# Optimization experiments

Measured on AMD Instinct MI355X. Metric: run time of the kernel, lower is better.

## Reference

```python
import jax, jax.numpy as jnp
import numpy as np

DIM = 768
H = 64
W = 64
NB = 8
BS = DIM // NB
LAMBD = 0.01
SCALE = 0.02


def softshrink(x, lambd):
    return jnp.sign(x) * jnp.maximum(jnp.abs(x) - lambd, 0.0)


def setup_inputs() -> dict:
    key = jax.random.key(0)
    ks = jax.random.split(key, 7)
    x = jax.random.normal(ks[0], (8, H * W, DIM), dtype=jnp.float32)
    w1 = SCALE * jax.random.normal(ks[1], (2, NB, BS, BS), dtype=jnp.float32)
    b1 = SCALE * jax.random.normal(ks[2], (2, NB, BS), dtype=jnp.float32)
    w2 = SCALE * jax.random.normal(ks[3], (2, NB, BS, BS), dtype=jnp.float32)
    b2 = SCALE * jax.random.normal(ks[4], (2, NB, BS), dtype=jnp.float32)
    # Conv1d(dim, dim, kernel_size=1) == per-token linear: weight [C_out, C_in], bias [C_out]
    Wb = (1.0 / np.sqrt(DIM)) * jax.random.normal(ks[5], (DIM, DIM), dtype=jnp.float32)
    bb = (1.0 / np.sqrt(DIM)) * jax.random.normal(ks[6], (DIM,), dtype=jnp.float32)
    return {"x": x, "w1": w1, "b1": b1, "w2": w2, "b2": b2, "Wb": Wb, "bb": bb}


def reference(x, w1, b1, w2, b2, Wb, bb):
    B, N, C = x.shape
    # bias path: Conv1d with kernel 1 is a linear map over channels
    bias = jnp.einsum('bnc,dc->bnd', x, Wb) + bb
    # spectral path
    xg = x.reshape(B, H, W, C)
    xf = jnp.fft.rfft2(xg, axes=(1, 2), norm='ortho')          # [B, H, W//2+1, C] complex64
    xf = xf.reshape(B, H, W // 2 + 1, NB, BS)
    xr, xi = jnp.real(xf), jnp.imag(xf)
    # layer 1: complex block-diagonal matmul + relu
    r1 = jax.nn.relu(jnp.einsum('...bd,bdk->...bk', xr, w1[0])
                     - jnp.einsum('...bd,bdk->...bk', xi, w1[1]) + b1[0])
    i1 = jax.nn.relu(jnp.einsum('...bd,bdk->...bk', xr, w1[1])
                     + jnp.einsum('...bd,bdk->...bk', xi, w1[0]) + b1[1])
    # layer 2
    r2 = (jnp.einsum('...bd,bdk->...bk', r1, w2[0])
          - jnp.einsum('...bd,bdk->...bk', i1, w2[1]) + b2[0])
    i2 = (jnp.einsum('...bd,bdk->...bk', r1, w2[1])
          + jnp.einsum('...bd,bdk->...bk', i1, w2[0]) + b2[1])
    r2 = softshrink(r2, LAMBD)
    i2 = softshrink(i2, LAMBD)
    xc = (r2 + 1j * i2).reshape(B, H, W // 2 + 1, C)
    xo = jnp.fft.irfft2(xc, s=(H, W), axes=(1, 2), norm='ortho')  # [B, H, W, C]
    return xo.reshape(B, N, C) + bias
```

## Files before the change

kernel.cpp:

```cpp
#include <hip/hip_runtime.h>
#include <math.h>

#ifndef M_PI
#define M_PI 3.14159265358979323846
#endif

namespace {

constexpr int kDim = 768;
constexpr int kNKW = 33;
constexpr int kB = 8;
constexpr float kLambd = 0.01f;
constexpr size_t kXFElems = (size_t)kB * kNKW * 64 * kDim;

typedef __attribute__((ext_vector_type(8))) __bf16 bf16x8;
typedef __attribute__((ext_vector_type(8))) short short8;
typedef __attribute__((ext_vector_type(4))) float f32x4;

alignas(16) __device__ unsigned short g_wT[4 * 8 * 96 * 96];
alignas(16) __device__ unsigned short g_twC[64 * 64];
alignas(16) __device__ unsigned short g_twS[64 * 64];
alignas(16) __device__ unsigned short g_iwC[64 * 64];
alignas(16) __device__ unsigned short g_iwS[64 * 64];

__device__ inline unsigned short f2bf(float f) {
  unsigned int u = __float_as_uint(f);
  unsigned int r = (u + 0x7FFFu + ((u >> 16) & 1u)) >> 16;
  return (unsigned short)r;
}

__device__ inline bf16x8 s2b(short8 s) { return __builtin_bit_cast(bf16x8, s); }
__device__ inline bf16x8 negb(short8 s) {
  s ^= (short)0x8000;
  return __builtin_bit_cast(bf16x8, s);
}

__device__ inline void gload_lds16(const void* g, void* l) {
  __builtin_amdgcn_global_load_lds(
      (const __attribute__((address_space(1))) unsigned int*)g,
      (__attribute__((address_space(3))) unsigned int*)l, 16, 0, 0);
}

__global__ __launch_bounds__(256) void init_tables_kernel() {
  const int e = blockIdx.x * 256 + threadIdx.x;
  if (e >= 4096) return;
  const int a = e >> 6;
  const int bcol = e & 63;
  const float ang = (float)(2.0 * M_PI / 64.0) * (float)((a * bcol) & 63);
  float s_, c_;
  __sincosf(ang, &s_, &c_);
  g_twC[e] = f2bf(0.125f * c_);
  g_twS[e] = f2bf(0.125f * s_);
  unsigned short cv = 0, sv = 0;
  if (bcol < 33) {
    const float al = (bcol == 0 || bcol == 32) ? 0.125f : 0.25f;
    cv = f2bf(al * c_);
    sv = f2bf(-al * s_);
  }
  g_iwC[e] = cv;
  g_iwS[e] = sv;
}

__global__ __launch_bounds__(256) void cvt_f32_bf16_kernel(
    const float* __restrict__ in, unsigned short* __restrict__ out, int n4) {
  int i = blockIdx.x * 256 + threadIdx.x;
  if (i >= n4) return;
  const float4 v = reinterpret_cast<const float4*>(in)[i];
  ushort4 o;
  o.x = f2bf(v.x); o.y = f2bf(v.y); o.z = f2bf(v.z); o.w = f2bf(v.w);
  reinterpret_cast<ushort4*>(out)[i] = o;
}

__global__ __launch_bounds__(256) void cvt_w_kernel(
    const float* __restrict__ w1, const float* __restrict__ w2) {
  const int e = blockIdx.x * 256 + threadIdx.x;
  if (e >= 4 * 8 * 96 * 96) return;
  const int k = e % 96;
  const int d = (e / 96) % 96;
  const int nbm = e / 9216;
  const int mtx = nbm >> 3;
  const int nb = nbm & 7;
  const float* src =
      (mtx < 2 ? w1 : w2) + ((size_t)(mtx & 1) * 8 + nb) * 9216;
  g_wT[((size_t)nbm * 96 + k) * 96 + d] = f2bf(src[d * 96 + k]);
}

__global__ __launch_bounds__(256) void mfma_gemm_kernel(
    const unsigned short* __restrict__ xbf, const unsigned short* __restrict__ wbf,
    const float* __restrict__ bb, float* __restrict__ out) {
  __shared__ unsigned short As[128 * 32];
  __shared__ unsigned short Bs[128 * 32];
  const int t = threadIdx.x;
  const int lane = t & 63;
  const int wid = t >> 6;
  const int wm = wid >> 1;
  const int wn = wid & 1;
  const int id = blockIdx.x;
  const int swz = (id & 7) * 192 + (id >> 3);
  const int m0 = (swz / 6) * 128;
  const int n0 = (swz % 6) * 128;

  f32x4 acc[4][4];
#pragma unroll
  for (int i = 0; i < 4; ++i)
#pragma unroll
    for (int j = 0; j < 4; ++j) acc[i][j] = (f32x4){0.f, 0.f, 0.f, 0.f};

  char* AsB = (char*)As;
  char* BsB = (char*)Bs;
  const int cl = lane & 15;
  const int kg = lane >> 4;

  for (int k0 = 0; k0 < 768; k0 += 32) {
#pragma unroll
    for (int i = 0; i < 2; ++i) {
      const int off = (wid * 2 + i) * 1024 + lane * 16;
      const int row = off >> 6;
      const int kb = off & 63;
      const char* gA = (const char*)xbf + ((size_t)(m0 + row) * 768 + k0) * 2 + kb;
      gload_lds16(gA, AsB + (wid * 2 + i) * 1024);
      const char* gB = (const char*)wbf + ((size_t)(n0 + row) * 768 + k0) * 2 + kb;
      gload_lds16(gB, BsB + (wid * 2 + i) * 1024);
    }
    asm volatile("s_waitcnt vmcnt(0)" ::: "memory");
    __syncthreads();

    bf16x8 av[4], bv[4];
#pragma unroll
    for (int mi = 0; mi < 4; ++mi) {
      const int r = wm * 64 + mi * 16 + cl;
      av[mi] = *reinterpret_cast<const bf16x8*>(AsB + r * 64 + kg * 16);
    }
#pragma unroll
    for (int ni = 0; ni < 4; ++ni) {
      const int r = wn * 64 + ni * 16 + cl;
      bv[ni] = *reinterpret_cast<const bf16x8*>(BsB + r * 64 + kg * 16);
    }
#pragma unroll
    for (int mi = 0; mi < 4; ++mi)
#pragma unroll
      for (int ni = 0; ni < 4; ++ni)
        acc[mi][ni] = __builtin_amdgcn_mfma_f32_16x16x32_bf16(
            av[mi], bv[ni], acc[mi][ni], 0, 0, 0);
    __syncthreads();
  }

#pragma unroll
  for (int ni = 0; ni < 4; ++ni) {
    const int n = n0 + wn * 64 + ni * 16 + cl;
    const float bias = bb[n];
#pragma unroll
    for (int mi = 0; mi < 4; ++mi) {
      const int m = m0 + wm * 64 + mi * 16 + kg * 4;
#pragma unroll
      for (int r = 0; r < 4; ++r) {
        out[(size_t)(m + r) * 768 + n] = acc[mi][ni][r] + bias;
      }
    }
  }
}

__global__ __launch_bounds__(256) void rfft_row_mfma_kernel(
    const float* __restrict__ x, unsigned short* __restrict__ xbf,
    unsigned short* __restrict__ XFr, unsigned short* __restrict__ XFi) {
  __shared__ alignas(16) unsigned short Cs[48 * 80];
  __shared__ alignas(16) unsigned short Ss[48 * 80];
  __shared__ alignas(16) unsigned short xs[64 * 66];
  const int t = threadIdx.x;
  for (int e = t; e < 48 * 64; e += 256) {
    const int kh = e >> 6;
    const int w = e & 63;
    const float ang = (float)(2.0 * M_PI / 64.0) * (float)((kh * w) & 63);
    float s_, c_;
    __sincosf(ang, &s_, &c_);
    Cs[kh * 80 + w] = f2bf(0.125f * c_);
    Ss[kh * 80 + w] = f2bf(-0.125f * s_);
  }

  const int lane = t & 63;
  const int wv = t >> 6;
  const int cl = lane & 15;
  const int kg = lane >> 4;
  const int bh = blockIdx.x;
  const int b = bh >> 6;
  const int h = bh & 63;
  const int c0 = blockIdx.y * 64;

  {
    const float* xrow = x + (size_t)bh * (64 * 768) + c0;
    unsigned short* xbrow = xbf + (size_t)bh * (64 * 768) + c0;
    const int wofs = lane >> 5;
    const int c2 = (lane & 31) * 2;
#pragma unroll
    for (int it = 0; it < 8; ++it) {
      const int w = wv * 16 + it * 2 + wofs;
      const float2 v = *reinterpret_cast<const float2*>(xrow + (size_t)w * 768 + c2);
      ushort2 bv;
      bv.x = f2bf(v.x);
      bv.y = f2bf(v.y);
      *reinterpret_cast<ushort2*>(xbrow + (size_t)w * 768 + c2) = bv;
      *reinterpret_cast<ushort2*>(xs + w * 66 + c2) = bv;
    }
  }
  __syncthreads();

  const int cA = wv * 16 + cl;
  short8 ax[2];
#pragma unroll
  for (int kf = 0; kf < 2; ++kf) {
#pragma unroll
    for (int j = 0; j < 8; ++j)
      ax[kf][j] = (short)xs[(kf * 32 + kg * 8 + j) * 66 + cA];
  }

  f32x4 aR[3], aI[3];
#pragma unroll
  for (int nt = 0; nt < 3; ++nt) {
    aR[nt] = (f32x4){0.f, 0.f, 0.f, 0.f};
    aI[nt] = (f32x4){0.f, 0.f, 0.f, 0.f};
  }

#pragma unroll
  for (int nt = 0; nt < 3; ++nt) {
#pragma unroll
    for (int kf = 0; kf < 2; ++kf) {
      const int row = nt * 16 + cl;
      const int w0 = kf * 32 + kg * 8;
      const bf16x8 bc = *reinterpret_cast<const bf16x8*>(Cs + row * 80 + w0);
      const bf16x8 bs = *reinterpret_cast<const bf16x8*>(Ss + row * 80 + w0);
      aR[nt] = __builtin_amdgcn_mfma_f32_16x16x32_bf16(s2b(ax[kf]), bc, aR[nt], 0, 0, 0);
      aI[nt] = __builtin_amdgcn_mfma_f32_16x16x32_bf16(s2b(ax[kf]), bs, aI[nt], 0, 0, 0);
    }
  }

  const int cD = c0 + wv * 16 + kg * 4;
#pragma unroll
  for (int nt = 0; nt < 3; ++nt) {
    const int kh = nt * 16 + cl;
    if (kh <= 32) {
      const size_t off = (((size_t)b * kNKW + kh) * 64 + h) * 768 + cD;
      ushort4 vr, vi;
      vr.x = f2bf(aR[nt][0]); vr.y = f2bf(aR[nt][1]);
      vr.z = f2bf(aR[nt][2]); vr.w = f2bf(aR[nt][3]);
      vi.x = f2bf(aI[nt][0]); vi.y = f2bf(aI[nt][1]);
      vi.z = f2bf(aI[nt][2]); vi.w = f2bf(aI[nt][3]);
      *reinterpret_cast<ushort4*>(XFr + off) = vr;
      *reinterpret_cast<ushort4*>(XFi + off) = vi;
    }
  }
}

__global__ __launch_bounds__(256) void spectral_mid_kernel(
    unsigned short* __restrict__ Xr, unsigned short* __restrict__ Xi,
    const float* __restrict__ b1, const float* __restrict__ b2) {
  __shared__ alignas(16) unsigned short sXr[64 * 104];
  __shared__ alignas(16) unsigned short sXi[64 * 104];
  __shared__ alignas(16) unsigned short sYr[64 * 104];
  __shared__ alignas(16) unsigned short sYi[64 * 104];
  const int t = threadIdx.x;
  const int lane = t & 63;
  const int wid = t >> 6;
  const int wm = wid >> 1;
  const int wn = wid & 1;
  const int cl = lane & 15;
  const int kg = lane >> 4;
  const int nb = blockIdx.y;
  const size_t gbase = (size_t)blockIdx.x * (64 * 768) + nb * 96;

  short8 pcs[2][2], pss[2][2];
#pragma unroll
  for (int mt = 0; mt < 2; ++mt) {
#pragma unroll
    for (int kf = 0; kf < 2; ++kf) {
      const int row = wm * 32 + mt * 16 + cl;
      const int k0 = kf * 32 + kg * 8;
      pcs[mt][kf] = *reinterpret_cast<const short8*>(g_twC + row * 64 + k0);
      pss[mt][kf] = *reinterpret_cast<const short8*>(g_twS + row * 64 + k0);
    }
  }

  {
    const int row = t >> 2;
    const int q = t & 3;
    const size_t gof = gbase + (size_t)row * 768 + q * 24;
    unsigned short* lr = sXr + row * 104 + q * 24;
    unsigned short* li = sXi + row * 104 + q * 24;
#pragma unroll
    for (int v = 0; v < 3; ++v) {
      *reinterpret_cast<short8*>(lr + v * 8) =
          *reinterpret_cast<const short8*>(Xr + gof + v * 8);
      *reinterpret_cast<short8*>(li + v * 8) =
          *reinterpret_cast<const short8*>(Xi + gof + v * 8);
    }
  }
  __syncthreads();

  f32x4 accR[2][3], accI[2][3];

#pragma unroll
  for (int mt = 0; mt < 2; ++mt)
#pragma unroll
    for (int nt = 0; nt < 3; ++nt) {
      accR[mt][nt] = (f32x4){0.f, 0.f, 0.f, 0.f};
      accI[mt][nt] = (f32x4){0.f, 0.f, 0.f, 0.f};
    }
#pragma unroll
  for (int kf = 0; kf < 2; ++kf) {
    const int k0 = kf * 32 + kg * 8;
    short8 bR[3], bI[3];
#pragma unroll
    for (int nt = 0; nt < 3; ++nt) {
      const int col = wn * 48 + nt * 16 + cl;
#pragma unroll
      for (int j = 0; j < 8; ++j) {
        bR[nt][j] = (short)sXr[(k0 + j) * 104 + col];
        bI[nt][j] = (short)sXi[(k0 + j) * 104 + col];
      }
    }
#pragma unroll
    for (int mt = 0; mt < 2; ++mt) {
      const short8 cs = pcs[mt][kf];
      const short8 ss = pss[mt][kf];
#pragma unroll
      for (int nt = 0; nt < 3; ++nt) {
        accR[mt][nt] = __builtin_amdgcn_mfma_f32_16x16x32_bf16(s2b(cs), s2b(bR[nt]), accR[mt][nt], 0, 0, 0);
        accR[mt][nt] = __builtin_amdgcn_mfma_f32_16x16x32_bf16(s2b(ss), s2b(bI[nt]), accR[mt][nt], 0, 0, 0);
        accI[mt][nt] = __builtin_amdgcn_mfma_f32_16x16x32_bf16(s2b(cs), s2b(bI[nt]), accI[mt][nt], 0, 0, 0);
        accI[mt][nt] = __builtin_amdgcn_mfma_f32_16x16x32_bf16(negb(ss), s2b(bR[nt]), accI[mt][nt], 0, 0, 0);
      }
    }
  }
#pragma unroll
  for (int mt = 0; mt < 2; ++mt) {
#pragma unroll
    for (int nt = 0; nt < 3; ++nt) {
      const int col = wn * 48 + nt * 16 + cl;
      const int row0 = wm * 32 + mt * 16 + kg * 4;
#pragma unroll
      for (int r = 0; r < 4; ++r) {
        sYr[(row0 + r) * 104 + col] = f2bf(accR[mt][nt][r]);
        sYi[(row0 + r) * 104 + col] = f2bf(accI[mt][nt][r]);
      }
    }
  }
  __syncthreads();

  const unsigned short* wt1r = g_wT + (size_t)(0 * 8 + nb) * 9216;
  const unsigned short* wt1i = g_wT + (size_t)(1 * 8 + nb) * 9216;
  const unsigned short* wt2r = g_wT + (size_t)(2 * 8 + nb) * 9216;
  const unsigned short* wt2i = g_wT + (size_t)(3 * 8 + nb) * 9216;

#pragma unroll
  for (int mt = 0; mt < 2; ++mt)
#pragma unroll
    for (int nt = 0; nt < 3; ++nt) {
      accR[mt][nt] = (f32x4){0.f, 0.f, 0.f, 0.f};
      accI[mt][nt] = (f32x4){0.f, 0.f, 0.f, 0.f};
    }
#pragma unroll
  for (int kk = 0; kk < 3; ++kk) {
    const int ko = kk * 32 + kg * 8;
    short8 axr[2], axi[2];
#pragma unroll
    for (int mt = 0; mt < 2; ++mt) {
      const int row = wm * 32 + mt * 16 + cl;
      axr[mt] = *reinterpret_cast<const short8*>(sYr + row * 104 + ko);
      axi[mt] = *reinterpret_cast<const short8*>(sYi + row * 104 + ko);
    }
    short8 wr_[3], wi_[3];
#pragma unroll
    for (int nt = 0; nt < 3; ++nt) {
      const int rw = wn * 48 + nt * 16 + cl;
      wr_[nt] = *reinterpret_cast<const short8*>(wt1r + rw * 96 + ko);
      wi_[nt] = *reinterpret_cast<const short8*>(wt1i + rw * 96 + ko);
    }
#pragma unroll
    for (int mt = 0; mt < 2; ++mt) {
      const bf16x8 ar = s2b(axr[mt]);
      const bf16x8 ai = s2b(axi[mt]);
      const bf16x8 ain = negb(axi[mt]);
#pragma unroll
      for (int nt = 0; nt < 3; ++nt) {
        accR[mt][nt] = __builtin_amdgcn_mfma_f32_16x16x32_bf16(ar, s2b(wr_[nt]), accR[mt][nt], 0, 0, 0);
        accR[mt][nt] = __builtin_amdgcn_mfma_f32_16x16x32_bf16(ain, s2b(wi_[nt]), accR[mt][nt], 0, 0, 0);
        accI[mt][nt] = __builtin_amdgcn_mfma_f32_16x16x32_bf16(ar, s2b(wi_[nt]), accI[mt][nt], 0, 0, 0);
        accI[mt][nt] = __builtin_amdgcn_mfma_f32_16x16x32_bf16(ai, s2b(wr_[nt]), accI[mt][nt], 0, 0, 0);
      }
    }
  }
#pragma unroll
  for (int nt = 0; nt < 3; ++nt) {
    const int col = wn * 48 + nt * 16 + cl;
    const float br = b1[nb * 96 + col];
    const float bi = b1[768 + nb * 96 + col];
#pragma unroll
    for (int mt = 0; mt < 2; ++mt) {
      const int row0 = wm * 32 + mt * 16 + kg * 4;
#pragma unroll
      for (int r = 0; r < 4; ++r) {
        sXr[(row0 + r) * 104 + col] = f2bf(fmaxf(accR[mt][nt][r] + br, 0.f));
        sXi[(row0 + r) * 104 + col] = f2bf(fmaxf(accI[mt][nt][r] + bi, 0.f));
      }
    }
  }
  __syncthreads();

#pragma unroll
  for (int mt = 0; mt < 2; ++mt)
#pragma unroll
    for (int nt = 0; nt < 3; ++nt) {
      accR[mt][nt] = (f32x4){0.f, 0.f, 0.f, 0.f};
      accI[mt][nt] = (f32x4){0.f, 0.f, 0.f, 0.f};
    }
#pragma unroll
  for (int kk = 0; kk < 3; ++kk) {
    const int ko = kk * 32 + kg * 8;
    short8 axr[2], axi[2];
#pragma unroll
    for (int mt = 0; mt < 2; ++mt) {
      const int row = wm * 32 + mt * 16 + cl;
      axr[mt] = *reinterpret_cast<const short8*>(sXr + row * 104 + ko);
      axi[mt] = *reinterpret_cast<const short8*>(sXi + row * 104 + ko);
    }
    short8 wr_[3], wi_[3];
#pragma unroll
    for (int nt = 0; nt < 3; ++nt) {
      const int rw = wn * 48 + nt * 16 + cl;
      wr_[nt] = *reinterpret_cast<const short8*>(wt2r + rw * 96 + ko);
      wi_[nt] = *reinterpret_cast<const short8*>(wt2i + rw * 96 + ko);
    }
#pragma unroll
    for (int mt = 0; mt < 2; ++mt) {
      const bf16x8 ar = s2b(axr[mt]);
      const bf16x8 ai = s2b(axi[mt]);
      const bf16x8 ain = negb(axi[mt]);
#pragma unroll
      for (int nt = 0; nt < 3; ++nt) {
        accR[mt][nt] = __builtin_amdgcn_mfma_f32_16x16x32_bf16(ar, s2b(wr_[nt]), accR[mt][nt], 0, 0, 0);
        accR[mt][nt] = __builtin_amdgcn_mfma_f32_16x16x32_bf16(ain, s2b(wi_[nt]), accR[mt][nt], 0, 0, 0);
        accI[mt][nt] = __builtin_amdgcn_mfma_f32_16x16x32_bf16(ar, s2b(wi_[nt]), accI[mt][nt], 0, 0, 0);
        accI[mt][nt] = __builtin_amdgcn_mfma_f32_16x16x32_bf16(ai, s2b(wr_[nt]), accI[mt][nt], 0, 0, 0);
      }
    }
  }
#pragma unroll
  for (int nt = 0; nt < 3; ++nt) {
    const int col = wn * 48 + nt * 16 + cl;
    const float br = b2[nb * 96 + col];
    const float bi = b2[768 + nb * 96 + col];
#pragma unroll
    for (int mt = 0; mt < 2; ++mt) {
      const int row0 = wm * 32 + mt * 16 + kg * 4;
#pragma unroll
      for (int r = 0; r < 4; ++r) {
        float vr = accR[mt][nt][r] + br;
        float vi = accI[mt][nt][r] + bi;
        vr = (vr > kLambd) ? (vr - kLambd) : ((vr < -kLambd) ? (vr + kLambd) : 0.f);
        vi = (vi > kLambd) ? (vi - kLambd) : ((vi < -kLambd) ? (vi + kLambd) : 0.f);
        sYr[(row0 + r) * 104 + col] = f2bf(vr);
        sYi[(row0 + r) * 104 + col] = f2bf(vi);
      }
    }
  }
  __syncthreads();

#pragma unroll
  for (int mt = 0; mt < 2; ++mt)
#pragma unroll
    for (int nt = 0; nt < 3; ++nt) {
      accR[mt][nt] = (f32x4){0.f, 0.f, 0.f, 0.f};
      accI[mt][nt] = (f32x4){0.f, 0.f, 0.f, 0.f};
    }
#pragma unroll
  for (int kf = 0; kf < 2; ++kf) {
    const int k0 = kf * 32 + kg * 8;
    short8 bR[3], bI[3];
#pragma unroll
    for (int nt = 0; nt < 3; ++nt) {
      const int col = wn * 48 + nt * 16 + cl;
#pragma unroll
      for (int j = 0; j < 8; ++j) {
        bR[nt][j] = (short)sYr[(k0 + j) * 104 + col];
        bI[nt][j] = (short)sYi[(k0 + j) * 104 + col];
      }
    }
#pragma unroll
    for (int mt = 0; mt < 2; ++mt) {
      const short8 cs = pcs[mt][kf];
      const short8 ss = pss[mt][kf];
#pragma unroll
      for (int nt = 0; nt < 3; ++nt) {
        accR[mt][nt] = __builtin_amdgcn_mfma_f32_16x16x32_bf16(s2b(cs), s2b(bR[nt]), accR[mt][nt], 0, 0, 0);
        accR[mt][nt] = __builtin_amdgcn_mfma_f32_16x16x32_bf16(negb(ss), s2b(bI[nt]), accR[mt][nt], 0, 0, 0);
        accI[mt][nt] = __builtin_amdgcn_mfma_f32_16x16x32_bf16(s2b(cs), s2b(bI[nt]), accI[mt][nt], 0, 0, 0);
        accI[mt][nt] = __builtin_amdgcn_mfma_f32_16x16x32_bf16(s2b(ss), s2b(bR[nt]), accI[mt][nt], 0, 0, 0);
      }
    }
  }
#pragma unroll
  for (int mt = 0; mt < 2; ++mt) {
#pragma unroll
    for (int nt = 0; nt < 3; ++nt) {
      const int col = wn * 48 + nt * 16 + cl;
      const int row0 = wm * 32 + mt * 16 + kg * 4;
#pragma unroll
      for (int r = 0; r < 4; ++r) {
        const size_t off = gbase + (size_t)(row0 + r) * 768 + col;
        Xr[off] = f2bf(accR[mt][nt][r]);
        Xi[off] = f2bf(accI[mt][nt][r]);
      }
    }
  }
}

__global__ __launch_bounds__(256) void irfft_row_add_mfma_kernel(
    const unsigned short* __restrict__ Zr, const unsigned short* __restrict__ Zi,
    float* __restrict__ out) {
  const int t = threadIdx.x;
  const int lane = t & 63;
  const int wv = t >> 6;
  const int cl = lane & 15;
  const int kg = lane >> 4;
  const int bh = blockIdx.x;
  const int b = bh >> 6;
  const int h = bh & 63;
  const int cb = blockIdx.y * 64 + wv * 16;

  short8 pbc[4][2], pbs[4][2];
#pragma unroll
  for (int nt = 0; nt < 4; ++nt) {
#pragma unroll
    for (int kf = 0; kf < 2; ++kf) {
      const int row = nt * 16 + cl;
      const int kw0 = kf * 32 + kg * 8;
      pbc[nt][kf] = *reinterpret_cast<const short8*>(g_iwC + row * 64 + kw0);
      pbs[nt][kf] = *reinterpret_cast<const short8*>(g_iwS + row * 64 + kw0);
    }
  }

  const int cA = cb + cl;
  short8 azr[2], azi[2];
#pragma unroll
  for (int kf = 0; kf < 2; ++kf) {
#pragma unroll
    for (int j = 0; j < 8; ++j) {
      const int kw = kf * 32 + kg * 8 + j;
      short zr = 0, zi = 0;
      if (kw < 33) {
        const size_t off = (((size_t)b * kNKW + kw) * 64 + h) * 768 + cA;
        zr = (short)Zr[off];
        zi = (short)Zi[off];
      }
      azr[kf][j] = zr;
      azi[kf][j] = zi;
    }
  }

  const int cD = cb + kg * 4;
  float* obase = out + ((size_t)bh * 64) * 768;
  f32x4 aO[4];
#pragma unroll
  for (int nt = 0; nt < 4; ++nt) {
    const int w = nt * 16 + cl;
    aO[nt] = *reinterpret_cast<const f32x4*>(obase + (size_t)w * 768 + cD);
  }

#pragma unroll
  for (int nt = 0; nt < 4; ++nt) {
#pragma unroll
    for (int kf = 0; kf < 2; ++kf) {
      aO[nt] = __builtin_amdgcn_mfma_f32_16x16x32_bf16(s2b(azr[kf]), s2b(pbc[nt][kf]), aO[nt], 0, 0, 0);
      aO[nt] = __builtin_amdgcn_mfma_f32_16x16x32_bf16(s2b(azi[kf]), s2b(pbs[nt][kf]), aO[nt], 0, 0, 0);
    }
  }

#pragma unroll
  for (int nt = 0; nt < 4; ++nt) {
    const int w = nt * 16 + cl;
    *reinterpret_cast<f32x4*>(obase + (size_t)w * 768 + cD) = aO[nt];
  }
}

}

extern "C" void kernel_launch(void* const* d_in, const int* in_sizes, int n_in,
                              void* d_out, int out_size, void* d_ws,
                              size_t ws_size, hipStream_t stream) {
  (void)in_sizes; (void)n_in; (void)out_size;
  const float* x  = (const float*)d_in[0];
  const float* w1 = (const float*)d_in[1];
  const float* b1 = (const float*)d_in[2];
  const float* w2 = (const float*)d_in[3];
  const float* b2 = (const float*)d_in[4];
  const float* Wb = (const float*)d_in[5];
  const float* bb = (const float*)d_in[6];
  float* out = (float*)d_out;

  if (ws_size < 2 * kXFElems * sizeof(float)) return;
  unsigned short* xbf = (unsigned short*)d_ws;
  unsigned short* wbf = xbf + (size_t)32768 * 768;
  unsigned short* XFr = wbf + (size_t)768 * 768;
  unsigned short* XFi = XFr + kXFElems;

  init_tables_kernel<<<dim3(16), 256, 0, stream>>>();
  cvt_f32_bf16_kernel<<<dim3((768 * 768 / 4 + 255) / 256), 256, 0, stream>>>(
      Wb, wbf, 768 * 768 / 4);
  cvt_w_kernel<<<dim3(4 * 8 * 96 * 96 / 256), 256, 0, stream>>>(w1, w2);
  rfft_row_mfma_kernel<<<dim3(512, 12), 256, 0, stream>>>(x, xbf, XFr, XFi);
  mfma_gemm_kernel<<<dim3(1536), 256, 0, stream>>>(xbf, wbf, bb, out);
  spectral_mid_kernel<<<dim3(264, 8), 256, 0, stream>>>(XFr, XFi, b1, b2);
  irfft_row_add_mfma_kernel<<<dim3(512, 12), 256, 0, stream>>>(XFr, XFi, out);
}
```

Baseline: 245.1 us.

## Double-buffer GEMM LDS tiles and halve spectral kernel shared memory

```diff
diff --git a/kernel.cpp b/kernel.cpp
--- a/kernel.cpp
+++ b/kernel.cpp
@@ -88,8 +88,8 @@
 __global__ __launch_bounds__(256) void mfma_gemm_kernel(
     const unsigned short* __restrict__ xbf, const unsigned short* __restrict__ wbf,
     const float* __restrict__ bb, float* __restrict__ out) {
-  __shared__ unsigned short As[128 * 32];
-  __shared__ unsigned short Bs[128 * 32];
+  __shared__ unsigned short As[2][128 * 32];
+  __shared__ unsigned short Bs[2][128 * 32];
   const int t = threadIdx.x;
   const int lane = t & 63;
   const int wid = t >> 6;
@@ -106,12 +106,12 @@
 #pragma unroll
     for (int j = 0; j < 4; ++j) acc[i][j] = (f32x4){0.f, 0.f, 0.f, 0.f};
 
-  char* AsB = (char*)As;
-  char* BsB = (char*)Bs;
   const int cl = lane & 15;
   const int kg = lane >> 4;
 
-  for (int k0 = 0; k0 < 768; k0 += 32) {
+  auto stage = [&](int buf, int k0) {
+    char* AsB = (char*)As[buf];
+    char* BsB = (char*)Bs[buf];
 #pragma unroll
     for (int i = 0; i < 2; ++i) {
       const int off = (wid * 2 + i) * 1024 + lane * 16;
@@ -122,9 +122,18 @@
       const char* gB = (const char*)wbf + ((size_t)(n0 + row) * 768 + k0) * 2 + kb;
       gload_lds16(gB, BsB + (wid * 2 + i) * 1024);
     }
-    asm volatile("s_waitcnt vmcnt(0)" ::: "memory");
-    __syncthreads();
-
+  };
+
+  stage(0, 0);
+  asm volatile("s_waitcnt vmcnt(0)" ::: "memory");
+  __syncthreads();
+
+  for (int tstep = 0; tstep < 24; ++tstep) {
+    const int buf = tstep & 1;
+    if (tstep + 1 < 24) stage(buf ^ 1, (tstep + 1) * 32);
+
+    const char* AsB = (const char*)As[buf];
+    const char* BsB = (const char*)Bs[buf];
     bf16x8 av[4], bv[4];
 #pragma unroll
     for (int mi = 0; mi < 4; ++mi) {
@@ -142,6 +151,8 @@
       for (int ni = 0; ni < 4; ++ni)
         acc[mi][ni] = __builtin_amdgcn_mfma_f32_16x16x32_bf16(
             av[mi], bv[ni], acc[mi][ni], 0, 0, 0);
+
+    asm volatile("s_waitcnt vmcnt(0)" ::: "memory");
     __syncthreads();
   }
 
@@ -253,10 +264,8 @@
 __global__ __launch_bounds__(256) void spectral_mid_kernel(
     unsigned short* __restrict__ Xr, unsigned short* __restrict__ Xi,
     const float* __restrict__ b1, const float* __restrict__ b2) {
-  __shared__ alignas(16) unsigned short sXr[64 * 104];
-  __shared__ alignas(16) unsigned short sXi[64 * 104];
-  __shared__ alignas(16) unsigned short sYr[64 * 104];
-  __shared__ alignas(16) unsigned short sYi[64 * 104];
+  __shared__ alignas(16) unsigned short sR[64 * 104];
+  __shared__ alignas(16) unsigned short sI[64 * 104];
   const int t = threadIdx.x;
   const int lane = t & 63;
   const int wid = t >> 6;
@@ -283,8 +292,8 @@
     const int row = t >> 2;
     const int q = t & 3;
     const size_t gof = gbase + (size_t)row * 768 + q * 24;
-    unsigned short* lr = sXr + row * 104 + q * 24;
-    unsigned short* li = sXi + row * 104 + q * 24;
+    unsigned short* lr = sR + row * 104 + q * 24;
+    unsigned short* li = sI + row * 104 + q * 24;
 #pragma unroll
     for (int v = 0; v < 3; ++v) {
       *reinterpret_cast<short8*>(lr + v * 8) =
@@ -313,8 +322,8 @@
       const int col = wn * 48 + nt * 16 + cl;
 #pragma unroll
       for (int j = 0; j < 8; ++j) {
-        bR[nt][j] = (short)sXr[(k0 + j) * 104 + col];
-        bI[nt][j] = (short)sXi[(k0 + j) * 104 + col];
+        bR[nt][j] = (short)sR[(k0 + j) * 104 + col];
+        bI[nt][j] = (short)sI[(k0 + j) * 104 + col];
       }
     }
 #pragma unroll
@@ -330,6 +339,7 @@
       }
     }
   }
+  __syncthreads();
 #pragma unroll
   for (int mt = 0; mt < 2; ++mt) {
 #pragma unroll
@@ -338,8 +348,8 @@
       const int row0 = wm * 32 + mt * 16 + kg * 4;
 #pragma unroll
       for (int r = 0; r < 4; ++r) {
-        sYr[(row0 + r) * 104 + col] = f2bf(accR[mt][nt][r]);
-        sYi[(row0 + r) * 104 + col] = f2bf(accI[mt][nt][r]);
+        sR[(row0 + r) * 104 + col] = f2bf(accR[mt][nt][r]);
+        sI[(row0 + r) * 104 + col] = f2bf(accI[mt][nt][r]);
       }
     }
   }
@@ -364,8 +374,8 @@
 #pragma unroll
     for (int mt = 0; mt < 2; ++mt) {
       const int row = wm * 32 + mt * 16 + cl;
-      axr[mt] = *reinterpret_cast<const short8*>(sYr + row * 104 + ko);
-      axi[mt] = *reinterpret_cast<const short8*>(sYi + row * 104 + ko);
+      axr[mt] = *reinterpret_cast<const short8*>(sR + row * 104 + ko);
+      axi[mt] = *reinterpret_cast<const short8*>(sI + row * 104 + ko);
     }
     short8 wr_[3], wi_[3];
 #pragma unroll
@@ -388,6 +398,7 @@
       }
     }
   }
+  __syncthreads();
 #pragma unroll
   for (int nt = 0; nt < 3; ++nt) {
     const int col = wn * 48 + nt * 16 + cl;
@@ -398,8 +409,8 @@
       const int row0 = wm * 32 + mt * 16 + kg * 4;
 #pragma unroll
       for (int r = 0; r < 4; ++r) {
-        sXr[(row0 + r) * 104 + col] = f2bf(fmaxf(accR[mt][nt][r] + br, 0.f));
-        sXi[(row0 + r) * 104 + col] = f2bf(fmaxf(accI[mt][nt][r] + bi, 0.f));
+        sR[(row0 + r) * 104 + col] = f2bf(fmaxf(accR[mt][nt][r] + br, 0.f));
+        sI[(row0 + r) * 104 + col] = f2bf(fmaxf(accI[mt][nt][r] + bi, 0.f));
       }
     }
   }
@@ -419,8 +430,8 @@
 #pragma unroll
     for (int mt = 0; mt < 2; ++mt) {
       const int row = wm * 32 + mt * 16 + cl;
-      axr[mt] = *reinterpret_cast<const short8*>(sXr + row * 104 + ko);
-      axi[mt] = *reinterpret_cast<const short8*>(sXi + row * 104 + ko);
+      axr[mt] = *reinterpret_cast<const short8*>(sR + row * 104 + ko);
+      axi[mt] = *reinterpret_cast<const short8*>(sI + row * 104 + ko);
     }
     short8 wr_[3], wi_[3];
 #pragma unroll
@@ -443,6 +454,7 @@
       }
     }
   }
+  __syncthreads();
 #pragma unroll
   for (int nt = 0; nt < 3; ++nt) {
     const int col = wn * 48 + nt * 16 + cl;
@@ -457,8 +469,8 @@
         float vi = accI[mt][nt][r] + bi;
         vr = (vr > kLambd) ? (vr - kLambd) : ((vr < -kLambd) ? (vr + kLambd) : 0.f);
         vi = (vi > kLambd) ? (vi - kLambd) : ((vi < -kLambd) ? (vi + kLambd) : 0.f);
-        sYr[(row0 + r) * 104 + col] = f2bf(vr);
-        sYi[(row0 + r) * 104 + col] = f2bf(vi);
+        sR[(row0 + r) * 104 + col] = f2bf(vr);
+        sI[(row0 + r) * 104 + col] = f2bf(vi);
       }
     }
   }
@@ -480,8 +492,8 @@
       const int col = wn * 48 + nt * 16 + cl;
 #pragma unroll
       for (int j = 0; j < 8; ++j) {
-        bR[nt][j] = (short)sYr[(k0 + j) * 104 + col];
-        bI[nt][j] = (short)sYi[(k0 + j) * 104 + col];
+        bR[nt][j] = (short)sR[(k0 + j) * 104 + col];
+        bI[nt][j] = (short)sI[(k0 + j) * 104 + col];
       }
     }
 #pragma unroll
```

Result: no change. 248.3 us (+1.3%).

## Restructure spectral mid kernel with transposed LDS layouts and per-wave row tiles

Applied to the files above, without the earlier changes.

```diff
diff --git a/kernel.cpp b/kernel.cpp
--- a/kernel.cpp
+++ b/kernel.cpp
@@ -253,95 +253,76 @@
 __global__ __launch_bounds__(256) void spectral_mid_kernel(
     unsigned short* __restrict__ Xr, unsigned short* __restrict__ Xi,
     const float* __restrict__ b1, const float* __restrict__ b2) {
-  __shared__ alignas(16) unsigned short sXr[64 * 104];
-  __shared__ alignas(16) unsigned short sXi[64 * 104];
-  __shared__ alignas(16) unsigned short sYr[64 * 104];
-  __shared__ alignas(16) unsigned short sYi[64 * 104];
+  __shared__ alignas(16) unsigned short bR0[96 * 72];
+  __shared__ alignas(16) unsigned short bI0[96 * 72];
+  __shared__ alignas(16) unsigned short bR1[96 * 72];
+  __shared__ alignas(16) unsigned short bI1[96 * 72];
   const int t = threadIdx.x;
   const int lane = t & 63;
-  const int wid = t >> 6;
-  const int wm = wid >> 1;
-  const int wn = wid & 1;
+  const int wv = t >> 6;
   const int cl = lane & 15;
   const int kg = lane >> 4;
   const int nb = blockIdx.y;
   const size_t gbase = (size_t)blockIdx.x * (64 * 768) + nb * 96;
 
-  short8 pcs[2][2], pss[2][2];
-#pragma unroll
-  for (int mt = 0; mt < 2; ++mt) {
+  short8 pcs[2], pss[2];
+#pragma unroll
+  for (int kf = 0; kf < 2; ++kf) {
+    const int row = wv * 16 + cl;
+    const int k0 = kf * 32 + kg * 8;
+    pcs[kf] = *reinterpret_cast<const short8*>(g_twC + row * 64 + k0);
+    pss[kf] = *reinterpret_cast<const short8*>(g_twS + row * 64 + k0);
+  }
+
+  {
+    const int h = t >> 2;
+    const int q = t & 3;
+    const size_t gof = gbase + (size_t)h * 768 + q * 24;
+#pragma unroll
+    for (int v = 0; v < 3; ++v) {
+      const short8 vr = *reinterpret_cast<const short8*>(Xr + gof + v * 8);
+      const short8 vi = *reinterpret_cast<const short8*>(Xi + gof + v * 8);
+#pragma unroll
+      for (int e = 0; e < 8; ++e) {
+        const int c = q * 24 + v * 8 + e;
+        bR0[c * 72 + h] = (unsigned short)vr[e];
+        bI0[c * 72 + h] = (unsigned short)vi[e];
+      }
+    }
+  }
+  __syncthreads();
+
+  f32x4 accR[6], accI[6];
+
+#pragma unroll
+  for (int mt = 0; mt < 6; ++mt) {
+    accR[mt] = (f32x4){0.f, 0.f, 0.f, 0.f};
+    accI[mt] = (f32x4){0.f, 0.f, 0.f, 0.f};
+  }
+#pragma unroll
+  for (int mt = 0; mt < 6; ++mt) {
 #pragma unroll
     for (int kf = 0; kf < 2; ++kf) {
-      const int row = wm * 32 + mt * 16 + cl;
-      const int k0 = kf * 32 + kg * 8;
-      pcs[mt][kf] = *reinterpret_cast<const short8*>(g_twC + row * 64 + k0);
-      pss[mt][kf] = *reinterpret_cast<const short8*>(g_twS + row * 64 + k0);
-    }
-  }
-
-  {
-    const int row = t >> 2;
-    const int q = t & 3;
-    const size_t gof = gbase + (size_t)row * 768 + q * 24;
-    unsigned short* lr = sXr + row * 104 + q * 24;
-    unsigned short* li = sXi + row * 104 + q * 24;
-#pragma unroll
-    for (int v = 0; v < 3; ++v) {
-      *reinterpret_cast<short8*>(lr + v * 8) =
-          *reinterpret_cast<const short8*>(Xr + gof + v * 8);
-      *reinterpret_cast<short8*>(li + v * 8) =
-          *reinterpret_cast<const short8*>(Xi + gof + v * 8);
-    }
-  }
-  __syncthreads();
-
-  f32x4 accR[2][3], accI[2][3];
-
-#pragma unroll
-  for (int mt = 0; mt < 2; ++mt)
-#pragma unroll
-    for (int nt = 0; nt < 3; ++nt) {
-      accR[mt][nt] = (f32x4){0.f, 0.f, 0.f, 0.f};
-      accI[mt][nt] = (f32x4){0.f, 0.f, 0.f, 0.f};
-    }
-#pragma unroll
-  for (int kf = 0; kf < 2; ++kf) {
-    const int k0 = kf * 32 + kg * 8;
-    short8 bR[3], bI[3];
-#pragma unroll
-    for (int nt = 0; nt < 3; ++nt) {
-      const int col = wn * 48 + nt * 16 + cl;
-#pragma unroll
-      for (int j = 0; j < 8; ++j) {
-        bR[nt][j] = (short)sXr[(k0 + j) * 104 + col];
-        bI[nt][j] = (short)sXi[(k0 + j) * 104 + col];
-      }
-    }
-#pragma unroll
-    for (int mt = 0; mt < 2; ++mt) {
-      const short8 cs = pcs[mt][kf];
-      const short8 ss = pss[mt][kf];
-#pragma unroll
-      for (int nt = 0; nt < 3; ++nt) {
-        accR[mt][nt] = __builtin_amdgcn_mfma_f32_16x16x32_bf16(s2b(cs), s2b(bR[nt]), accR[mt][nt], 0, 0, 0);
-        accR[mt][nt] = __builtin_amdgcn_mfma_f32_16x16x32_bf16(s2b(ss), s2b(bI[nt]), accR[mt][nt], 0, 0, 0);
-        accI[mt][nt] = __builtin_amdgcn_mfma_f32_16x16x32_bf16(s2b(cs), s2b(bI[nt]), accI[mt][nt], 0, 0, 0);
-        accI[mt][nt] = __builtin_amdgcn_mfma_f32_16x16x32_bf16(negb(ss), s2b(bR[nt]), accI[mt][nt], 0, 0, 0);
-      }
-    }
-  }
-#pragma unroll
-  for (int mt = 0; mt < 2; ++mt) {
-#pragma unroll
-    for (int nt = 0; nt < 3; ++nt) {
-      const int col = wn * 48 + nt * 16 + cl;
-      const int row0 = wm * 32 + mt * 16 + kg * 4;
-#pragma unroll
-      for (int r = 0; r < 4; ++r) {
-        sYr[(row0 + r) * 104 + col] = f2bf(accR[mt][nt][r]);
-        sYi[(row0 + r) * 104 + col] = f2bf(accI[mt][nt][r]);
-      }
-    }
+      const int ro = (mt * 16 + cl) * 72 + kf * 32 + kg * 8;
+      const short8 axr = *reinterpret_cast<const short8*>(bR0 + ro);
+      const short8 axi = *reinterpret_cast<const short8*>(bI0 + ro);
+      accR[mt] = __builtin_amdgcn_mfma_f32_16x16x32_bf16(s2b(axr), s2b(pcs[kf]), accR[mt], 0, 0, 0);
+      accR[mt] = __builtin_amdgcn_mfma_f32_16x16x32_bf16(s2b(axi), s2b(pss[kf]), accR[mt], 0, 0, 0);
+      accI[mt] = __builtin_amdgcn_mfma_f32_16x16x32_bf16(s2b(axi), s2b(pcs[kf]), accI[mt], 0, 0, 0);
+      accI[mt] = __builtin_amdgcn_mfma_f32_16x16x32_bf16(negb(axr), s2b(pss[kf]), accI[mt], 0, 0, 0);
+    }
+  }
+#pragma unroll
+  for (int mt = 0; mt < 6; ++mt) {
+    const int kh = wv * 16 + cl;
+    const int c4 = mt * 16 + kg * 4;
+    ushort4 vr, vi;
+    vr.x = f2bf(accR[mt][0]); vr.y = f2bf(accR[mt][1]);
+    vr.z = f2bf(accR[mt][2]); vr.w = f2bf(accR[mt][3]);
+    vi.x = f2bf(accI[mt][0]); vi.y = f2bf(accI[mt][1]);
+    vi.z = f2bf(accI[mt][2]); vi.w = f2bf(accI[mt][3]);
+    *reinterpret_cast<ushort4*>(bR1 + kh * 104 + c4) = vr;
+    *reinterpret_cast<ushort4*>(bI1 + kh * 104 + c4) = vi;
   }
   __syncthreads();
 
@@ -351,165 +332,124 @@
   const unsigned short* wt2i = g_wT + (size_t)(3 * 8 + nb) * 9216;
 
 #pragma unroll
-  for (int mt = 0; mt < 2; ++mt)
-#pragma unroll
-    for (int nt = 0; nt < 3; ++nt) {
-      accR[mt][nt] = (f32x4){0.f, 0.f, 0.f, 0.f};
-      accI[mt][nt] = (f32x4){0.f, 0.f, 0.f, 0.f};
-    }
+  for (int nt = 0; nt < 6; ++nt) {
+    accR[nt] = (f32x4){0.f, 0.f, 0.f, 0.f};
+    accI[nt] = (f32x4){0.f, 0.f, 0.f, 0.f};
+  }
 #pragma unroll
   for (int kk = 0; kk < 3; ++kk) {
     const int ko = kk * 32 + kg * 8;
-    short8 axr[2], axi[2];
-#pragma unroll
-    for (int mt = 0; mt < 2; ++mt) {
-      const int row = wm * 32 + mt * 16 + cl;
-      axr[mt] = *reinterpret_cast<const short8*>(sYr + row * 104 + ko);
-      axi[mt] = *reinterpret_cast<const short8*>(sYi + row * 104 + ko);
-    }
-    short8 wr_[3], wi_[3];
-#pragma unroll
-    for (int nt = 0; nt < 3; ++nt) {
-      const int rw = wn * 48 + nt * 16 + cl;
-      wr_[nt] = *reinterpret_cast<const short8*>(wt1r + rw * 96 + ko);
-      wi_[nt] = *reinterpret_cast<const short8*>(wt1i + rw * 96 + ko);
-    }
-#pragma unroll
-    for (int mt = 0; mt < 2; ++mt) {
-      const bf16x8 ar = s2b(axr[mt]);
-      const bf16x8 ai = s2b(axi[mt]);
-      const bf16x8 ain = negb(axi[mt]);
-#pragma unroll
-      for (int nt = 0; nt < 3; ++nt) {
-        accR[mt][nt] = __builtin_amdgcn_mfma_f32_16x16x32_bf16(ar, s2b(wr_[nt]), accR[mt][nt], 0, 0, 0);
-        accR[mt][nt] = __builtin_amdgcn_mfma_f32_16x16x32_bf16(ain, s2b(wi_[nt]), accR[mt][nt], 0, 0, 0);
-        accI[mt][nt] = __builtin_amdgcn_mfma_f32_16x16x32_bf16(ar, s2b(wi_[nt]), accI[mt][nt], 0, 0, 0);
-        accI[mt][nt] = __builtin_amdgcn_mfma_f32_16x16x32_bf16(ai, s2b(wr_[nt]), accI[mt][nt], 0, 0, 0);
-      }
-    }
-  }
-#pragma unroll
-  for (int nt = 0; nt < 3; ++nt) {
-    const int col = wn * 48 + nt * 16 + cl;
+    const int ro = (wv * 16 + cl) * 104 + ko;
+    const short8 ayr = *reinterpret_cast<const short8*>(bR1 + ro);
+    const short8 ayi = *reinterpret_cast<const short8*>(bI1 + ro);
+    const bf16x8 ar = s2b(ayr);
+    const bf16x8 ai = s2b(ayi);
+    const bf16x8 ain = negb(ayi);
+#pragma unroll
+    for (int nt = 0; nt < 6; ++nt) {
+      const int rw = (nt * 16 + cl) * 96 + ko;
+      const bf16x8 wr_ = *reinterpret_cast<const bf16x8*>(wt1r + rw);
+      const bf16x8 wi_ = *reinterpret_cast<const bf16x8*>(wt1i + rw);
+      accR[nt] = __builtin_amdgcn_mfma_f32_16x16x32_bf16(ar, wr_, accR[nt], 0, 0, 0);
+      accR[nt] = __builtin_amdgcn_mfma_f32_16x16x32_bf16(ain, wi_, accR[nt], 0, 0, 0);
+      accI[nt] = __builtin_amdgcn_mfma_f32_16x16x32_bf16(ar, wi_, accI[nt], 0, 0, 0);
+      accI[nt] = __builtin_amdgcn_mfma_f32_16x16x32_bf16(ai, wr_, accI[nt], 0, 0, 0);
+    }
+  }
+  __syncthreads();
+#pragma unroll
+  for (int nt = 0; nt < 6; ++nt) {
+    const int col = nt * 16 + cl;
     const float br = b1[nb * 96 + col];
     const float bi = b1[768 + nb * 96 + col];
 #pragma unroll
-    for (int mt = 0; mt < 2; ++mt) {
-      const int row0 = wm * 32 + mt * 16 + kg * 4;
-#pragma unroll
-      for (int r = 0; r < 4; ++r) {
-        sXr[(row0 + r) * 104 + col] = f2bf(fmaxf(accR[mt][nt][r] + br, 0.f));
-        sXi[(row0 + r) * 104 + col] = f2bf(fmaxf(accI[mt][nt][r] + bi, 0.f));
-      }
-    }
-  }
-  __syncthreads();
-
-#pragma unroll
-  for (int mt = 0; mt < 2; ++mt)
-#pragma unroll
-    for (int nt = 0; nt < 3; ++nt) {
-      accR[mt][nt] = (f32x4){0.f, 0.f, 0.f, 0.f};
-      accI[mt][nt] = (f32x4){0.f, 0.f, 0.f, 0.f};
-    }
+    for (int r = 0; r < 4; ++r) {
+      const int kh = wv * 16 + kg * 4 + r;
+      bR0[kh * 104 + col] = f2bf(fmaxf(accR[nt][r] + br, 0.f));
+      bI0[kh * 104 + col] = f2bf(fmaxf(accI[nt][r] + bi, 0.f));
+    }
+  }
+  __syncthreads();
+
+#pragma unroll
+  for (int nt = 0; nt < 6; ++nt) {
+    accR[nt] = (f32x4){0.f, 0.f, 0.f, 0.f};
+    accI[nt] = (f32x4){0.f, 0.f, 0.f, 0.f};
+  }
 #pragma unroll
   for (int kk = 0; kk < 3; ++kk) {
     const int ko = kk * 32 + kg * 8;
-    short8 axr[2], axi[2];
-#pragma unroll
-    for (int mt = 0; mt < 2; ++mt) {
-      const int row = wm * 32 + mt * 16 + cl;
-      axr[mt] = *reinterpret_cast<const short8*>(sXr + row * 104 + ko);
-      axi[mt] = *reinterpret_cast<const short8*>(sXi + row * 104 + ko);
-    }
-    short8 wr_[3], wi_[3];
-#pragma unroll
-    for (int nt = 0; nt < 3; ++nt) {
-      const int rw = wn * 48 + nt * 16 + cl;
-      wr_[nt] = *reinterpret_cast<const short8*>(wt2r + rw * 96 + ko);
-      wi_[nt] = *reinterpret_cast<const short8*>(wt2i + rw * 96 + ko);
-    }
-#pragma unroll
-    for (int mt = 0; mt < 2; ++mt) {
-      const bf16x8 ar = s2b(axr[mt]);
-      const bf16x8 ai = s2b(axi[mt]);
-      const bf16x8 ain = negb(axi[mt]);
-#pragma unroll
-      for (int nt = 0; nt < 3; ++nt) {
-        accR[mt][nt] = __builtin_amdgcn_mfma_f32_16x16x32_bf16(ar, s2b(wr_[nt]), accR[mt][nt], 0, 0, 0);
-        accR[mt][nt] = __builtin_amdgcn_mfma_f32_16x16x32_bf16(ain, s2b(wi_[nt]), accR[mt][nt], 0, 0, 0);
-        accI[mt][nt] = __builtin_amdgcn_mfma_f32_16x16x32_bf16(ar, s2b(wi_[nt]), accI[mt][nt], 0, 0, 0);
-        accI[mt][nt] = __builtin_amdgcn_mfma_f32_16x16x32_bf16(ai, s2b(wr_[nt]), accI[mt][nt], 0, 0, 0);
-      }
-    }
-  }
-#pragma unroll
-  for (int nt = 0; nt < 3; ++nt) {
-    const int col = wn * 48 + nt * 16 + cl;
+    const int ro = (wv * 16 + cl) * 104 + ko;
+    const short8 ayr = *reinterpret_cast<const short8*>(bR0 + ro);
+    const short8 ayi = *reinterpret_cast<const short8*>(bI0 + ro);
+    const bf16x8 ar = s2b(ayr);
+    const bf16x8 ai = s2b(ayi);
+    const bf16x8 ain = negb(ayi);
+#pragma unroll
+    for (int nt = 0; nt < 6; ++nt) {
+      const int rw = (nt * 16 + cl) * 96 + ko;
+      const bf16x8 wr_ = *reinterpret_cast<const bf16x8*>(wt2r + rw);
+      const bf16x8 wi_ = *reinterpret_cast<const bf16x8*>(wt2i + rw);
+      accR[nt] = __builtin_amdgcn_mfma_f32_16x16x32_bf16(ar, wr_, accR[nt], 0, 0, 0);
+      accR[nt] = __builtin_amdgcn_mfma_f32_16x16x32_bf16(ain, wi_, accR[nt], 0, 0, 0);
+      accI[nt] = __builtin_amdgcn_mfma_f32_16x16x32_bf16(ar, wi_, accI[nt], 0, 0, 0);
+      accI[nt] = __builtin_amdgcn_mfma_f32_16x16x32_bf16(ai, wr_, accI[nt], 0, 0, 0);
+    }
+  }
+  __syncthreads();
+#pragma unroll
+  for (int nt = 0; nt < 6; ++nt) {
+    const int col = nt * 16 + cl;
     const float br = b2[nb * 96 + col];
     const float bi = b2[768 + nb * 96 + col];
-#pragma unroll
-    for (int mt = 0; mt < 2; ++mt) {
-      const int row0 = wm * 32 + mt * 16 + kg * 4;
-#pragma unroll
-      for (int r = 0; r < 4; ++r) {
-        float vr = accR[mt][nt][r] + br;
-        float vi = accI[mt][nt][r] + bi;
-        vr = (vr > kLambd) ? (vr - kLambd) : ((vr < -kLambd) ? (vr + kLambd) : 0.f);
-        vi = (vi > kLambd) ? (vi - kLambd) : ((vi < -kLambd) ? (vi + kLambd) : 0.f);
-        sYr[(row0 + r) * 104 + col] = f2bf(vr);
-        sYi[(row0 + r) * 104 + col] = f2bf(vi);
-      }
-    }
-  }
-  __syncthreads();
-
-#pragma unroll
-  for (int mt = 0; mt < 2; ++mt)
-#pragma unroll
-    for (int nt = 0; nt < 3; ++nt) {
-      accR[mt][nt] = (f32x4){0.f, 0.f, 0.f, 0.f};
-      accI[mt][nt] = (f32x4){0.f, 0.f, 0.f, 0.f};
-    }
-#pragma unroll
-  for (int kf = 0; kf < 2; ++kf) {
-    const int k0 = kf * 32 + kg * 8;
-    short8 bR[3], bI[3];
-#pragma unroll
-    for (int nt = 0; nt < 3; ++nt) {
-      const int col = wn * 48 + nt * 16 + cl;
-#pragma unroll
-      for (int j = 0; j < 8; ++j) {
-        bR[nt][j] = (short)sYr[(k0 + j) * 104 + col];
-        bI[nt][j] = (short)sYi[(k0 + j) * 104 + col];
-      }
-    }
-#pragma unroll
-    for (int mt = 0; mt < 2; ++mt) {
-      const short8 cs = pcs[mt][kf];
-      const short8 ss = pss[mt][kf];
-#pragma unroll
-      for (int nt = 0; nt < 3; ++nt) {
-        accR[mt][nt] = __builtin_amdgcn_mfma_f32_16x16x32_bf16(s2b(cs), s2b(bR[nt]), accR[mt][nt], 0, 0, 0);
-        accR[mt][nt] = __builtin_amdgcn_mfma_f32_16x16x32_bf16(negb(ss), s2b(bI[nt]), accR[mt][nt], 0, 0, 0);
-        accI[mt][nt] = __builtin_amdgcn_mfma_f32_16x16x32_bf16(s2b(cs), s2b(bI[nt]), accI[mt][nt], 0, 0, 0);
-        accI[mt][nt] = __builtin_amdgcn_mfma_f32_16x16x32_bf16(s2b(ss), s2b(bR[nt]), accI[mt][nt], 0, 0, 0);
-      }
-    }
-  }
-#pragma unroll
-  for (int mt = 0; mt < 2; ++mt) {
-#pragma unroll
-    for (int nt = 0; nt < 3; ++nt) {
-      const int col = wn * 48 + nt * 16 + cl;
-      const int row0 = wm * 32 + mt * 16 + kg * 4;
-#pragma unroll
-      for (int r = 0; r < 4; ++r) {
-        const size_t off = gbase + (size_t)(row0 + r) * 768 + col;
-        Xr[off] = f2bf(accR[mt][nt][r]);
-        Xi[off] = f2bf(accI[mt][nt][r]);
-      }
-    }
+    float pr[4], pi[4];
+#pragma unroll
+    for (int r = 0; r < 4; ++r) {
+      float vr = accR[nt][r] + br;
+      float vi = accI[nt][r] + bi;
+      vr = (vr > kLambd) ? (vr - kLambd) : ((vr < -kLambd) ? (vr + kLambd) : 0.f);
+      vi = (vi > kLambd) ? (vi - kLambd) : ((vi < -kLambd) ? (vi + kLambd) : 0.f);
+      pr[r] = vr; pi[r] = vi;
+    }
+    const int kh4 = wv * 16 + kg * 4;
+    ushort4 vr4, vi4;
+    vr4.x = f2bf(pr[0]); vr4.y = f2bf(pr[1]); vr4.z = f2bf(pr[2]); vr4.w = f2bf(pr[3]);
+    vi4.x = f2bf(pi[0]); vi4.y = f2bf(pi[1]); vi4.z = f2bf(pi[2]); vi4.w = f2bf(pi[3]);
+    *reinterpret_cast<ushort4*>(bR1 + col * 72 + kh4) = vr4;
+    *reinterpret_cast<ushort4*>(bI1 + col * 72 + kh4) = vi4;
+  }
+  __syncthreads();
+
+#pragma unroll
+  for (int mt = 0; mt < 6; ++mt) {
+    accR[mt] = (f32x4){0.f, 0.f, 0.f, 0.f};
+    accI[mt] = (f32x4){0.f, 0.f, 0.f, 0.f};
+  }
+#pragma unroll
+  for (int mt = 0; mt < 6; ++mt) {
+#pragma unroll
+    for (int kf = 0; kf < 2; ++kf) {
+      const int ro = (mt * 16 + cl) * 72 + kf * 32 + kg * 8;
+      const short8 ayr = *reinterpret_cast<const short8*>(bR1 + ro);
+      const short8 ayi = *reinterpret_cast<const short8*>(bI1 + ro);
+      accR[mt] = __builtin_amdgcn_mfma_f32_16x16x32_bf16(s2b(ayr), s2b(pcs[kf]), accR[mt], 0, 0, 0);
+      accR[mt] = __builtin_amdgcn_mfma_f32_16x16x32_bf16(negb(ayi), s2b(pss[kf]), accR[mt], 0, 0, 0);
+      accI[mt] = __builtin_amdgcn_mfma_f32_16x16x32_bf16(s2b(ayi), s2b(pcs[kf]), accI[mt], 0, 0, 0);
+      accI[mt] = __builtin_amdgcn_mfma_f32_16x16x32_bf16(s2b(ayr), s2b(pss[kf]), accI[mt], 0, 0, 0);
+    }
+  }
+#pragma unroll
+  for (int mt = 0; mt < 6; ++mt) {
+    const int h = wv * 16 + cl;
+    const int c4 = mt * 16 + kg * 4;
+    const size_t off = gbase + (size_t)h * 768 + c4;
+    ushort4 vr, vi;
+    vr.x = f2bf(accR[mt][0]); vr.y = f2bf(accR[mt][1]);
+    vr.z = f2bf(accR[mt][2]); vr.w = f2bf(accR[mt][3]);
+    vi.x = f2bf(accI[mt][0]); vi.y = f2bf(accI[mt][1]);
+    vi.z = f2bf(accI[mt][2]); vi.w = f2bf(accI[mt][3]);
+    *reinterpret_cast<ushort4*>(Xr + off) = vr;
+    *reinterpret_cast<ushort4*>(Xi + off) = vi;
   }
 }
 
```

Measured after the change: 272.1 us. 1.11x slower.
